# Kernel optimization log

Measured on AMD Instinct MI355X. Metric: run time of the kernel, lower is better.

The kernel has to match this reference:

```python
import math
import jax, jax.numpy as jnp
import numpy as np

N, E = 20000, 640000
S_DIM, Z_DIM, H, QK, VD = 64, 64, 4, 8, 8
EPS = 1e-8


def quat_rotate(v, q):
    # v: [..., 3], q: [..., 4] (w, x, y, z), broadcastable. Unit-quaternion rotation:
    # v' = v + 2*(w*(u x v) + u x (u x v))
    w = q[..., 0:1]
    u = q[..., 1:4]
    uv = jnp.cross(u, v)
    return v + 2.0 * (w * uv + jnp.cross(u, uv))


def setup_inputs() -> dict:
    key = jax.random.key(0)
    ks = jax.random.split(key, 16)
    s = jax.random.normal(ks[0], (N, S_DIM), dtype=jnp.float32)
    z = jax.random.normal(ks[1], (E, Z_DIM), dtype=jnp.float32)
    edge_index = jax.random.randint(ks[2], (2, E), 0, N)
    quaternion = jax.random.normal(ks[3], (N, 4), dtype=jnp.float32)
    quaternion = quaternion / jnp.linalg.norm(quaternion, axis=-1, keepdims=True)
    translation = jax.random.normal(ks[4], (N, 3), dtype=jnp.float32)
    sc_s = 1.0 / math.sqrt(S_DIM)
    sc_z = 1.0 / math.sqrt(Z_DIM)
    # weights stored [in, out] so y = x @ W (equivalent to torch x @ W.T)
    Wq_s = jax.random.normal(ks[5], (S_DIM, H * S_DIM), dtype=jnp.float32) * sc_s
    Wk_s = jax.random.normal(ks[6], (S_DIM, H * S_DIM), dtype=jnp.float32) * sc_s
    Wv_s = jax.random.normal(ks[7], (S_DIM, H * S_DIM), dtype=jnp.float32) * sc_s
    Wq_v = jax.random.normal(ks[8], (S_DIM, H * QK * 3), dtype=jnp.float32) * sc_s
    Wk_v = jax.random.normal(ks[9], (S_DIM, H * QK * 3), dtype=jnp.float32) * sc_s
    Wv_v = jax.random.normal(ks[10], (S_DIM, H * VD * 3), dtype=jnp.float32) * sc_s
    Wb = jax.random.normal(ks[11], (Z_DIM, H), dtype=jnp.float32) * sc_z
    bb = jnp.zeros((H,), dtype=jnp.float32)
    Wdz = jax.random.normal(ks[12], (Z_DIM, Z_DIM // 4), dtype=jnp.float32) * sc_z
    bdz = jnp.zeros((Z_DIM // 4,), dtype=jnp.float32)
    head_weights = jnp.full((H,), 0.541324854612918, dtype=jnp.float32)  # softplus^{-1}(1)
    concat_dim = Z_DIM // 4 + S_DIM + VD * 4
    Wout = jax.random.normal(ks[13], (H * concat_dim, S_DIM), dtype=jnp.float32) / math.sqrt(H * concat_dim)
    bout = jnp.zeros((S_DIM,), dtype=jnp.float32)
    return {
        's': s, 'z': z, 'edge_index': edge_index, 'quaternion': quaternion,
        'translation': translation, 'Wq_s': Wq_s, 'Wk_s': Wk_s, 'Wv_s': Wv_s,
        'Wq_v': Wq_v, 'Wk_v': Wk_v, 'Wv_v': Wv_v, 'Wb': Wb, 'bb': bb,
        'Wdz': Wdz, 'bdz': bdz, 'head_weights': head_weights,
        'Wout': Wout, 'bout': bout,
    }


def reference(s, z, edge_index, quaternion, translation,
              Wq_s, Wk_s, Wv_s, Wq_v, Wk_v, Wv_v,
              Wb, bb, Wdz, bdz, head_weights, Wout, bout):
    idx_i, idx_j = edge_index[0], edge_index[1]
    n = s.shape[0]
    h = head_weights.shape[0]
    qk = Wq_v.shape[1] // (3 * h)
    vd = Wv_v.shape[1] // (3 * h)

    q_scalar = (s @ Wq_s).reshape(n, h, -1)
    k_scalar = (s @ Wk_s).reshape(n, h, -1)
    v_scalar = (s @ Wv_s).reshape(n, h, -1)

    def to_points(x):
        # torch.split into 3 chunks then stack(dim=-1): [n, 3*c] -> [n, c, 3]
        c = x.shape[-1] // 3
        return jnp.swapaxes(x.reshape(n, 3, c), 1, 2)

    quat_b = quaternion[:, None, :]
    trans_b = translation[:, None, :]
    q_vec = (quat_rotate(to_points(s @ Wq_v), quat_b) + trans_b).reshape(n, h, qk, 3)
    k_vec = (quat_rotate(to_points(s @ Wk_v), quat_b) + trans_b).reshape(n, h, qk, 3)
    v_vec = (quat_rotate(to_points(s @ Wv_v), quat_b) + trans_b).reshape(n, h, vd, 3)

    b_bias = z @ Wb + bb  # [E, H]

    attn = jnp.sum(k_scalar[idx_i] * q_scalar[idx_j], axis=-1)  # [E, H]
    attn = attn * math.sqrt(1.0 / 3 * qk) + math.sqrt(1.0 / 3) * b_bias

    disp = q_vec[idx_i] - k_vec[idx_j]            # [E, H, qk, 3]
    vec_att = jnp.sum(disp * disp, axis=-1)       # [E, H, qk]
    hw = jax.nn.softplus(head_weights)[None, :, None]
    vec_att = jnp.sum(vec_att * hw, axis=-1) * math.sqrt(1.0 / (3 * (qk * 9.0 / 2))) * (-0.5)
    attn = attn + vec_att

    # segment softmax over destination node idx_i
    seg_max = jax.ops.segment_max(attn, idx_i, num_segments=n)
    ea = jnp.exp(attn - seg_max[idx_i])
    denom = jax.ops.segment_sum(ea, idx_i, num_segments=n)
    attn = ea / denom[idx_i]                      # [E, H]

    out_scalar = jax.ops.segment_sum(attn[:, :, None] * v_scalar[idx_i], idx_i, num_segments=n)
    out_scalar = out_scalar.reshape(n, -1)

    out_vec = jax.ops.segment_sum(attn[:, :, None, None] * v_vec[idx_i], idx_i, num_segments=n)
    out_vec = out_vec - translation[:, None, None, :]
    q_conj = jnp.concatenate([quaternion[:, :1], -quaternion[:, 1:]], axis=-1)
    out_vec = quat_rotate(out_vec, q_conj[:, None, None, :])   # [n, h, vd, 3]
    out_vec_norm = jnp.sqrt(jnp.sum(out_vec * out_vec, axis=-1) + EPS).reshape(n, -1)
    out_vec_flat = out_vec.reshape(n, -1, 3)

    pair_z = z @ Wdz + bdz                         # [E, z/4]
    out_pair = jax.ops.segment_sum(attn[:, :, None] * pair_z[:, None, :], idx_i, num_segments=n)
    out_pair = out_pair.reshape(n, -1)

    feats = jnp.concatenate([out_scalar,
                             out_vec_flat[..., 0], out_vec_flat[..., 1], out_vec_flat[..., 2],
                             out_vec_norm, out_pair], axis=-1)
    return feats @ Wout + bout
```

## Files before the change

### kernel.cpp

```cpp
#include <hip/hip_runtime.h>
#include <stdint.h>


#define C_SQRT83  1.6329931618554518f
#define C_SQRT13  0.5773502691896258f
#define C_VEC    -0.04811252243246881f

__device__ __forceinline__ unsigned short f2bf(float f){
  unsigned u = __float_as_uint(f);
  u += 0x7fffu + ((u >> 16) & 1u);
  return (unsigned short)(u >> 16);
}
__device__ __forceinline__ unsigned pack2(float a, float b){
  return (unsigned)f2bf(a) | ((unsigned)f2bf(b) << 16);
}
__device__ __forceinline__ float bflo(unsigned u){ return __uint_as_float(u << 16); }
__device__ __forceinline__ float bfhi(unsigned u){ return __uint_as_float(u & 0xffff0000u); }

__device__ __forceinline__ void quat_rot(float w, float ux, float uy, float uz,
                                         float vx, float vy, float vz,
                                         float& ox, float& oy, float& oz){
  float cx = uy*vz - uz*vy;
  float cy = uz*vx - ux*vz;
  float cz = ux*vy - uy*vx;
  float dx = uy*cz - uz*cy;
  float dy = uz*cx - ux*cz;
  float dz = ux*cy - uy*cx;
  ox = vx + 2.f*(w*cx + dx);
  oy = vy + 2.f*(w*cy + dy);
  oz = vz + 2.f*(w*cz + dz);
}


__global__ __launch_bounds__(256) void k_zero(unsigned* __restrict__ counts, int n){
  int g = blockIdx.x*256 + threadIdx.x;
  if (g < n) counts[g] = 0u;
}

__global__ __launch_bounds__(256) void k_count(const int* __restrict__ ei,
                                               unsigned* __restrict__ counts, int ne){
  int e = blockIdx.x*256 + threadIdx.x;
  if (e >= ne) return;
  atomicAdd(&counts[ei[e]], 1u);
}

__global__ __launch_bounds__(256) void k_scan(const unsigned* __restrict__ counts,
                                              unsigned* __restrict__ row_off,
                                              unsigned* __restrict__ cursor, int n){
  __shared__ unsigned part[256];
  int t = threadIdx.x;
  int chunk = (n + 255) >> 8;
  int s0 = t*chunk, s1 = min(s0 + chunk, n);
  unsigned sum = 0;
  for (int k = s0; k < s1; ++k) sum += counts[k];
  part[t] = sum; __syncthreads();
  for (int off = 1; off < 256; off <<= 1){
    unsigned v = (t >= off) ? part[t-off] : 0u;
    __syncthreads();
    part[t] += v;
    __syncthreads();
  }
  unsigned run = (t == 0) ? 0u : part[t-1];
  for (int k = s0; k < s1; ++k){
    row_off[k] = run; cursor[k] = run; run += counts[k];
  }
  if (t == 255) row_off[n] = part[255];
}

__global__ __launch_bounds__(256) void k_fill(const int* __restrict__ ei,
                                              unsigned* __restrict__ cursor,
                                              unsigned* __restrict__ si,
                                              unsigned* __restrict__ sj,
                                              unsigned* __restrict__ se, int ne){
  int e = blockIdx.x*256 + threadIdx.x;
  if (e >= ne) return;
  int i = ei[e];
  unsigned pos = atomicAdd(&cursor[i], 1u);
  si[pos] = (unsigned)i;
  sj[pos] = (unsigned)ei[ne + e];
  se[pos] = (unsigned)e;
}


#define BN 32

__device__ __forceinline__ void pass256(const float* __restrict__ W,
                                        const float st[BN][66], int cg, int sl,
                                        float acc[8][4]){
  #pragma unroll
  for (int i=0;i<8;i++){ acc[i][0]=0.f; acc[i][1]=0.f; acc[i][2]=0.f; acc[i][3]=0.f; }
  #pragma unroll 4
  for (int k = 0; k < 64; ++k){
    const float4 w = *(const float4*)(W + (size_t)k*256 + cg*4);
    #pragma unroll
    for (int i=0;i<8;i++){
      const float sv = st[sl*8+i][k];
      acc[i][0] += sv*w.x; acc[i][1] += sv*w.y; acc[i][2] += sv*w.z; acc[i][3] += sv*w.w;
    }
  }
}

__device__ __forceinline__ void pass96(const float* __restrict__ W,
                                       const float st[BN][66], int cgp, int slp,
                                       float acc[4][4]){
  #pragma unroll
  for (int i=0;i<4;i++){ acc[i][0]=0.f; acc[i][1]=0.f; acc[i][2]=0.f; acc[i][3]=0.f; }
  if (cgp >= 24) return;
  #pragma unroll 4
  for (int k = 0; k < 64; ++k){
    const float4 w = *(const float4*)(W + (size_t)k*96 + cgp*4);
    #pragma unroll
    for (int i=0;i<4;i++){
      const float sv = st[slp*4+i][k];
      acc[i][0] += sv*w.x; acc[i][1] += sv*w.y; acc[i][2] += sv*w.z; acc[i][3] += sv*w.w;
    }
  }
}

__global__ __launch_bounds__(256) void k_proj(
    const float* __restrict__ s, const float* __restrict__ quat, const float* __restrict__ trans,
    const float* __restrict__ Wqs, const float* __restrict__ Wks, const float* __restrict__ Wvs,
    const float* __restrict__ Wqv, const float* __restrict__ Wkv, const float* __restrict__ Wvv,
    unsigned* __restrict__ qs, unsigned* __restrict__ ks, float* __restrict__ vs,
    unsigned* __restrict__ qv, unsigned* __restrict__ kv, float* __restrict__ vv, int n)
{
  __shared__ float st[BN][66];
  __shared__ float pt[BN][97];
  const int tid = threadIdx.x;
  const int node0 = blockIdx.x * BN;

  #pragma unroll
  for (int r = 0; r < 2; ++r){
    const int idx = tid + r*256;
    const int nd = idx >> 4, c4 = idx & 15;
    const int g = node0 + nd;
    float4 v = make_float4(0.f,0.f,0.f,0.f);
    if (g < n) v = *(const float4*)(s + (size_t)g*64 + c4*4);
    st[nd][c4*4+0]=v.x; st[nd][c4*4+1]=v.y; st[nd][c4*4+2]=v.z; st[nd][c4*4+3]=v.w;
  }
  __syncthreads();

  const int cg = tid & 63, sl = tid >> 6;
  const int cgp = tid & 31, slp = tid >> 5;
  float acc[8][4];

  pass256(Wqs, st, cg, sl, acc);
  #pragma unroll
  for (int i=0;i<8;i++){
    const int g = node0 + sl*8 + i;
    if (g < n){
      uint2 u; u.x = pack2(acc[i][0],acc[i][1]); u.y = pack2(acc[i][2],acc[i][3]);
      *(uint2*)(qs + (size_t)g*128 + cg*2) = u;
    }
  }
  pass256(Wks, st, cg, sl, acc);
  #pragma unroll
  for (int i=0;i<8;i++){
    const int g = node0 + sl*8 + i;
    if (g < n){
      uint2 u; u.x = pack2(acc[i][0],acc[i][1]); u.y = pack2(acc[i][2],acc[i][3]);
      *(uint2*)(ks + (size_t)g*128 + cg*2) = u;
    }
  }
  pass256(Wvs, st, cg, sl, acc);
  #pragma unroll
  for (int i=0;i<8;i++){
    const int g = node0 + sl*8 + i;
    if (g < n){
      float4 f; f.x=acc[i][0]; f.y=acc[i][1]; f.z=acc[i][2]; f.w=acc[i][3];
      *(float4*)(vs + (size_t)g*256 + cg*4) = f;
    }
  }

  float pac[4][4];

  pass96(Wqv, st, cgp, slp, pac);
  __syncthreads();
  if (cgp < 24){
    #pragma unroll
    for (int i=0;i<4;i++){
      #pragma unroll
      for (int c=0;c<4;c++) pt[slp*4+i][cgp*4+c] = pac[i][c];
    }
  }
  __syncthreads();
  #pragma unroll
  for (int r = 0; r < 2; ++r){
    const int t2 = tid + r*256;
    const int nd = t2 >> 4, pp = t2 & 15;
    const int g = node0 + nd;
    if (g < n){
      const float4 q4 = *(const float4*)(quat + (size_t)g*4);
      const float tx = trans[(size_t)g*3], ty = trans[(size_t)g*3+1], tz = trans[(size_t)g*3+2];
      float x0,y0,z0,x1,y1,z1;
      quat_rot(q4.x,q4.y,q4.z,q4.w, pt[nd][2*pp],   pt[nd][32+2*pp],   pt[nd][64+2*pp],   x0,y0,z0);
      quat_rot(q4.x,q4.y,q4.z,q4.w, pt[nd][2*pp+1], pt[nd][32+2*pp+1], pt[nd][64+2*pp+1], x1,y1,z1);
      x0+=tx; y0+=ty; z0+=tz; x1+=tx; y1+=ty; z1+=tz;
      unsigned* d = qv + (size_t)g*48 + pp*3;
      d[0] = pack2(x0,y0); d[1] = pack2(z0,x1); d[2] = pack2(y1,z1);
    }
  }

  pass96(Wkv, st, cgp, slp, pac);
  __syncthreads();
  if (cgp < 24){
    #pragma unroll
    for (int i=0;i<4;i++){
      #pragma unroll
      for (int c=0;c<4;c++) pt[slp*4+i][cgp*4+c] = pac[i][c];
    }
  }
  __syncthreads();
  #pragma unroll
  for (int r = 0; r < 2; ++r){
    const int t2 = tid + r*256;
    const int nd = t2 >> 4, pp = t2 & 15;
    const int g = node0 + nd;
    if (g < n){
      const float4 q4 = *(const float4*)(quat + (size_t)g*4);
      const float tx = trans[(size_t)g*3], ty = trans[(size_t)g*3+1], tz = trans[(size_t)g*3+2];
      float x0,y0,z0,x1,y1,z1;
      quat_rot(q4.x,q4.y,q4.z,q4.w, pt[nd][2*pp],   pt[nd][32+2*pp],   pt[nd][64+2*pp],   x0,y0,z0);
      quat_rot(q4.x,q4.y,q4.z,q4.w, pt[nd][2*pp+1], pt[nd][32+2*pp+1], pt[nd][64+2*pp+1], x1,y1,z1);
      x0+=tx; y0+=ty; z0+=tz; x1+=tx; y1+=ty; z1+=tz;
      unsigned* d = kv + (size_t)g*48 + pp*3;
      d[0] = pack2(x0,y0); d[1] = pack2(z0,x1); d[2] = pack2(y1,z1);
    }
  }

  pass96(Wvv, st, cgp, slp, pac);
  __syncthreads();
  if (cgp < 24){
    #pragma unroll
    for (int i=0;i<4;i++){
      #pragma unroll
      for (int c=0;c<4;c++) pt[slp*4+i][cgp*4+c] = pac[i][c];
    }
  }
  __syncthreads();
  #pragma unroll
  for (int r = 0; r < 12; ++r){
    const int idx = tid + r*256;
    const int nd = idx / 96, col = idx - nd*96;
    const int g = node0 + nd;
    if (g < n) vv[(size_t)g*96 + col] = pt[nd][col];
  }
}


__global__ __launch_bounds__(256) void k_edge(
    const float* __restrict__ z,
    const unsigned* __restrict__ si, const unsigned* __restrict__ sj, const unsigned* __restrict__ se,
    const float* __restrict__ Wb,  const float* __restrict__ bb,
    const float* __restrict__ Wdz, const float* __restrict__ bdz,
    const float* __restrict__ hwts,
    const unsigned* __restrict__ qs, const unsigned* __restrict__ ks,
    const unsigned* __restrict__ qv, const unsigned* __restrict__ kv,
    float* __restrict__ logits, unsigned* __restrict__ pz, int ne)
{
  const int p = blockIdx.x*256 + threadIdx.x;
  if (p >= ne) return;
  const unsigned i = si[p], j = sj[p], e = se[p];

  float b4[4];  b4[0]=b4[1]=b4[2]=b4[3]=0.f;
  float pacc[16];
  #pragma unroll
  for (int c=0;c<16;c++) pacc[c]=0.f;
  const float* zr = z + (size_t)e*64;
  #pragma unroll
  for (int k4 = 0; k4 < 16; ++k4){
    const float4 zv = *(const float4*)(zr + 4*k4);
    #pragma unroll
    for (int kk = 0; kk < 4; ++kk){
      const int k = 4*k4 + kk;
      const float zk = (kk==0)?zv.x:((kk==1)?zv.y:((kk==2)?zv.z:zv.w));
      const float4 wb = *(const float4*)(Wb + k*4);
      b4[0]+=zk*wb.x; b4[1]+=zk*wb.y; b4[2]+=zk*wb.z; b4[3]+=zk*wb.w;
      const float* wd = Wdz + k*16;
      const float4 w0=*(const float4*)(wd), w1=*(const float4*)(wd+4),
                   w2=*(const float4*)(wd+8), w3=*(const float4*)(wd+12);
      pacc[ 0]+=zk*w0.x; pacc[ 1]+=zk*w0.y; pacc[ 2]+=zk*w0.z; pacc[ 3]+=zk*w0.w;
      pacc[ 4]+=zk*w1.x; pacc[ 5]+=zk*w1.y; pacc[ 6]+=zk*w1.z; pacc[ 7]+=zk*w1.w;
      pacc[ 8]+=zk*w2.x; pacc[ 9]+=zk*w2.y; pacc[10]+=zk*w2.z; pacc[11]+=zk*w2.w;
      pacc[12]+=zk*w3.x; pacc[13]+=zk*w3.y; pacc[14]+=zk*w3.z; pacc[15]+=zk*w3.w;
    }
  }
  #pragma unroll
  for (int c=0;c<16;c++) pacc[c] += bdz[c];
  { uint4 u0, u1;
    u0.x=pack2(pacc[0],pacc[1]);   u0.y=pack2(pacc[2],pacc[3]);
    u0.z=pack2(pacc[4],pacc[5]);   u0.w=pack2(pacc[6],pacc[7]);
    u1.x=pack2(pacc[8],pacc[9]);   u1.y=pack2(pacc[10],pacc[11]);
    u1.z=pack2(pacc[12],pacc[13]); u1.w=pack2(pacc[14],pacc[15]);
    uint4* d = (uint4*)(pz + (size_t)p*8);
    d[0]=u0; d[1]=u1; }

  const uint4* kr = (const uint4*)(ks + (size_t)i*128);
  const uint4* qr = (const uint4*)(qs + (size_t)j*128);
  float sdot[4];
  #pragma unroll
  for (int h = 0; h < 4; ++h){
    float acc = 0.f;
    #pragma unroll
    for (int c = 0; c < 8; ++c){
      const uint4 a = kr[h*8+c];
      const uint4 b = qr[h*8+c];
      acc += bflo(a.x)*bflo(b.x) + bfhi(a.x)*bfhi(b.x);
      acc += bflo(a.y)*bflo(b.y) + bfhi(a.y)*bfhi(b.y);
      acc += bflo(a.z)*bflo(b.z) + bfhi(a.z)*bfhi(b.z);
      acc += bflo(a.w)*bflo(b.w) + bfhi(a.w)*bfhi(b.w);
    }
    sdot[h] = acc;
  }

  const uint4* qvr = (const uint4*)(qv + (size_t)i*48);
  const uint4* kvr = (const uint4*)(kv + (size_t)j*48);
  float vsum[4];
  #pragma unroll
  for (int h = 0; h < 4; ++h){
    float acc = 0.f;
    #pragma unroll
    for (int c = 0; c < 3; ++c){
      const uint4 a = qvr[h*3+c];
      const uint4 b = kvr[h*3+c];
      float d;
      d = bflo(a.x)-bflo(b.x); acc += d*d;  d = bfhi(a.x)-bfhi(b.x); acc += d*d;
      d = bflo(a.y)-bflo(b.y); acc += d*d;  d = bfhi(a.y)-bfhi(b.y); acc += d*d;
      d = bflo(a.z)-bflo(b.z); acc += d*d;  d = bfhi(a.z)-bfhi(b.z); acc += d*d;
      d = bflo(a.w)-bflo(b.w); acc += d*d;  d = bfhi(a.w)-bfhi(b.w); acc += d*d;
    }
    vsum[h] = acc;
  }

  float4 lg;
  {
    float l[4];
    #pragma unroll
    for (int h = 0; h < 4; ++h){
      const float hw = log1pf(__expf(hwts[h]));
      l[h] = C_SQRT83*sdot[h] + C_SQRT13*(b4[h] + bb[h]) + C_VEC*hw*vsum[h];
    }
    lg.x=l[0]; lg.y=l[1]; lg.z=l[2]; lg.w=l[3];
  }
  *(float4*)(logits + (size_t)p*4) = lg;
}


__global__ __launch_bounds__(256) void k_soft(
    const float* __restrict__ logits, const unsigned* __restrict__ pz,
    const unsigned* __restrict__ row_off, float* __restrict__ out_pair, int n)
{
  const int t = blockIdx.x*256 + threadIdx.x;
  if (t >= n*4) return;
  const int i = t >> 2, h = t & 3;
  const int beg = (int)row_off[i], end = (int)row_off[i+1];

  float m = -3.4e38f;
  for (int p = beg; p < end; ++p) m = fmaxf(m, logits[(size_t)p*4 + h]);

  float ssum = 0.f;
  float acc[16];
  #pragma unroll
  for (int c=0;c<16;c++) acc[c]=0.f;

  for (int p = beg; p < end; ++p){
    const float w = __expf(logits[(size_t)p*4 + h] - m);
    ssum += w;
    const uint4* pr = (const uint4*)(pz + (size_t)p*8);
    const uint4 a = pr[0], b = pr[1];
    acc[ 0]+=w*bflo(a.x); acc[ 1]+=w*bfhi(a.x);
    acc[ 2]+=w*bflo(a.y); acc[ 3]+=w*bfhi(a.y);
    acc[ 4]+=w*bflo(a.z); acc[ 5]+=w*bfhi(a.z);
    acc[ 6]+=w*bflo(a.w); acc[ 7]+=w*bfhi(a.w);
    acc[ 8]+=w*bflo(b.x); acc[ 9]+=w*bfhi(b.x);
    acc[10]+=w*bflo(b.y); acc[11]+=w*bfhi(b.y);
    acc[12]+=w*bflo(b.z); acc[13]+=w*bfhi(b.z);
    acc[14]+=w*bflo(b.w); acc[15]+=w*bfhi(b.w);
  }
  const float inv = (end > beg) ? (1.f/ssum) : 0.f;
  float4* dst = (float4*)(out_pair + (size_t)i*64 + h*16);
  float4 o;
  o.x=acc[0]*inv;  o.y=acc[1]*inv;  o.z=acc[2]*inv;  o.w=acc[3]*inv;  dst[0]=o;
  o.x=acc[4]*inv;  o.y=acc[5]*inv;  o.z=acc[6]*inv;  o.w=acc[7]*inv;  dst[1]=o;
  o.x=acc[8]*inv;  o.y=acc[9]*inv;  o.z=acc[10]*inv; o.w=acc[11]*inv; dst[2]=o;
  o.x=acc[12]*inv; o.y=acc[13]*inv; o.z=acc[14]*inv; o.w=acc[15]*inv; dst[3]=o;
}


__global__ __launch_bounds__(256) void k_out(
    const float* __restrict__ vs, const float* __restrict__ vv,
    const float* __restrict__ out_pair, const unsigned* __restrict__ row_off,
    const float* __restrict__ quat, const float* __restrict__ trans,
    const float* __restrict__ Wout, const float* __restrict__ bout,
    float* __restrict__ out, int n)
{
  __shared__ float feats[32][448];
  __shared__ int degs[32];
  const int tid = threadIdx.x;
  const int node0 = blockIdx.x*32;

  if (tid < 32){
    const int g = node0 + tid;
    degs[tid] = (g < n) ? (int)(row_off[g+1] - row_off[g]) : 1;
  }
  __syncthreads();

  for (int x = tid; x < 32*256; x += 256){
    const int nd = x >> 8, c = x & 255;
    const int g = node0 + nd;
    feats[nd][c] = (g < n && degs[nd] > 0) ? vs[(size_t)g*256 + c] : 0.f;
  }
  for (int x = tid; x < 32*64; x += 256){
    const int nd = x >> 6, c = x & 63;
    const int g = node0 + nd;
    feats[nd][384 + c] = (g < n) ? out_pair[(size_t)g*64 + c] : 0.f;
  }
  for (int x = tid; x < 32*32; x += 256){
    const int nd = x >> 5, pt = x & 31;
    const int g = node0 + nd;
    float X=0.f, Y=0.f, Z=0.f;
    if (g < n){
      if (degs[nd] > 0){
        X = vv[(size_t)g*96 + pt];
        Y = vv[(size_t)g*96 + 32 + pt];
        Z = vv[(size_t)g*96 + 64 + pt];
      } else {
        const float4 q4 = *(const float4*)(quat + (size_t)g*4);
        const float tx = trans[(size_t)g*3], ty = trans[(size_t)g*3+1], tz = trans[(size_t)g*3+2];
        quat_rot(q4.x, -q4.y, -q4.z, -q4.w, -tx, -ty, -tz, X, Y, Z);
      }
    }
    feats[nd][256 + pt] = X;
    feats[nd][288 + pt] = Y;
    feats[nd][320 + pt] = Z;
    feats[nd][352 + pt] = sqrtf(X*X + Y*Y + Z*Z + 1e-8f);
  }
  __syncthreads();

  const int lane = tid & 63;
  const int wave = tid >> 6;
  float acc[8];
  #pragma unroll
  for (int q8=0;q8<8;q8++) acc[q8]=0.f;

  for (int k = 0; k < 448; ++k){
    const float wv = Wout[(size_t)k*64 + lane];
    #pragma unroll
    for (int q8 = 0; q8 < 8; ++q8)
      acc[q8] += feats[wave*8 + q8][k] * wv;
  }
  const float bo = bout[lane];
  #pragma unroll
  for (int q8 = 0; q8 < 8; ++q8){
    const int g = node0 + wave*8 + q8;
    if (g < n) out[(size_t)g*64 + lane] = acc[q8] + bo;
  }
}


extern "C" void kernel_launch(void* const* d_in, const int* in_sizes, int n_in,
                              void* d_out, int out_size, void* d_ws, size_t ws_size,
                              hipStream_t stream) {
  const float* s     = (const float*)d_in[0];
  const float* z     = (const float*)d_in[1];
  const int*   ei    = (const int*)  d_in[2];
  const float* quat  = (const float*)d_in[3];
  const float* trans = (const float*)d_in[4];
  const float* Wqs   = (const float*)d_in[5];
  const float* Wks   = (const float*)d_in[6];
  const float* Wvs   = (const float*)d_in[7];
  const float* Wqv   = (const float*)d_in[8];
  const float* Wkv   = (const float*)d_in[9];
  const float* Wvv   = (const float*)d_in[10];
  const float* Wb    = (const float*)d_in[11];
  const float* bb    = (const float*)d_in[12];
  const float* Wdz   = (const float*)d_in[13];
  const float* bdz   = (const float*)d_in[14];
  const float* hwts  = (const float*)d_in[15];
  const float* Wout  = (const float*)d_in[16];
  const float* bout  = (const float*)d_in[17];
  float* out = (float*)d_out;

  const int n  = in_sizes[0] / 64;
  const int ne = in_sizes[1] / 64;

  size_t off = 0;
  char* base = (char*)d_ws;
  auto take = [&](size_t bytes)->char* {
    char* p = base + off;
    off += (bytes + 255) & ~(size_t)255;
    return p;
  };
  unsigned* qs     = (unsigned*)take((size_t)n*512);
  unsigned* ks     = (unsigned*)take((size_t)n*512);
  unsigned* qvt    = (unsigned*)take((size_t)n*192);
  unsigned* kvt    = (unsigned*)take((size_t)n*192);
  float*    vs     = (float*)   take((size_t)n*1024);
  float*    vv     = (float*)   take((size_t)n*384);
  float*    logits = (float*)   take((size_t)ne*16);
  unsigned* pz     = (unsigned*)take((size_t)ne*32);
  unsigned* counts = (unsigned*)take((size_t)n*4);
  unsigned* roff   = (unsigned*)take((size_t)(n+1)*4);
  unsigned* cur    = (unsigned*)take((size_t)n*4);
  unsigned* si     = (unsigned*)take((size_t)ne*4);
  unsigned* sj     = (unsigned*)take((size_t)ne*4);
  unsigned* se     = (unsigned*)take((size_t)ne*4);
  float*    opair  = (float*)   take((size_t)n*256);
  (void)ws_size; (void)n_in; (void)out_size;

  const int gbE = (ne + 255) / 256;
  const int gbN = (n  + 255) / 256;

  k_zero <<<gbN, 256, 0, stream>>>(counts, n);
  k_count<<<gbE, 256, 0, stream>>>(ei, counts, ne);
  k_scan <<<1,   256, 0, stream>>>(counts, roff, cur, n);
  k_fill <<<gbE, 256, 0, stream>>>(ei, cur, si, sj, se, ne);
  k_proj <<<(n + BN - 1)/BN, 256, 0, stream>>>(s, quat, trans, Wqs, Wks, Wvs, Wqv, Wkv, Wvv,
                                               qs, ks, vs, qvt, kvt, vv, n);
  k_edge <<<gbE, 256, 0, stream>>>(z, si, sj, se, Wb, bb, Wdz, bdz, hwts,
                                   qs, ks, qvt, kvt, logits, pz, ne);
  k_soft <<<(n*4 + 255)/256, 256, 0, stream>>>(logits, pz, roff, opair, n);
  k_out  <<<(n + 31)/32, 256, 0, stream>>>(vs, vv, opair, roff, quat, trans,
                                           Wout, bout, out, n);
}
```

Measured before the change: 688.1 us.

## Fuse edge logits and segment softmax into one wave-per-node kernel

Replaces the per-edge logit kernel and the per-node softmax kernel with a single kernel where each wavefront handles one destination node. It computes edge logits and pair projections in registers and shared memory, then does an online softmax accumulation. This removes the global logits and pair buffers and the si array, and loads the node's own k/q-vec rows once into shared memory. It also transposes the shared-memory input tile in the projection kernel and vectorizes feature reads in the output kernel. The risks are load imbalance on high-degree nodes, underused waves on low-degree nodes, and reliance on __threadfence_block instead of a barrier for intra-wave shared-memory ordering.

```diff
diff --git a/kernel.cpp b/kernel.cpp
--- a/kernel.cpp
+++ b/kernel.cpp
@@ -69,14 +69,12 @@
 
 __global__ __launch_bounds__(256) void k_fill(const int* __restrict__ ei,
                                               unsigned* __restrict__ cursor,
-                                              unsigned* __restrict__ si,
                                               unsigned* __restrict__ sj,
                                               unsigned* __restrict__ se, int ne){
   int e = blockIdx.x*256 + threadIdx.x;
   if (e >= ne) return;
   int i = ei[e];
   unsigned pos = atomicAdd(&cursor[i], 1u);
-  si[pos] = (unsigned)i;
   sj[pos] = (unsigned)ei[ne + e];
   se[pos] = (unsigned)e;
 }
@@ -85,23 +83,28 @@
 #define BN 32
 
 __device__ __forceinline__ void pass256(const float* __restrict__ W,
-                                        const float st[BN][66], int cg, int sl,
+                                        const float stT[64][40], int cg, int sl,
                                         float acc[8][4]){
   #pragma unroll
   for (int i=0;i<8;i++){ acc[i][0]=0.f; acc[i][1]=0.f; acc[i][2]=0.f; acc[i][3]=0.f; }
   #pragma unroll 4
   for (int k = 0; k < 64; ++k){
-    const float4 w = *(const float4*)(W + (size_t)k*256 + cg*4);
-    #pragma unroll
-    for (int i=0;i<8;i++){
-      const float sv = st[sl*8+i][k];
-      acc[i][0] += sv*w.x; acc[i][1] += sv*w.y; acc[i][2] += sv*w.z; acc[i][3] += sv*w.w;
-    }
+    const float4 w  = *(const float4*)(W + (size_t)k*256 + cg*4);
+    const float4 n0 = *(const float4*)&stT[k][sl*8];
+    const float4 n1 = *(const float4*)&stT[k][sl*8+4];
+    acc[0][0]+=n0.x*w.x; acc[0][1]+=n0.x*w.y; acc[0][2]+=n0.x*w.z; acc[0][3]+=n0.x*w.w;
+    acc[1][0]+=n0.y*w.x; acc[1][1]+=n0.y*w.y; acc[1][2]+=n0.y*w.z; acc[1][3]+=n0.y*w.w;
+    acc[2][0]+=n0.z*w.x; acc[2][1]+=n0.z*w.y; acc[2][2]+=n0.z*w.z; acc[2][3]+=n0.z*w.w;
+    acc[3][0]+=n0.w*w.x; acc[3][1]+=n0.w*w.y; acc[3][2]+=n0.w*w.z; acc[3][3]+=n0.w*w.w;
+    acc[4][0]+=n1.x*w.x; acc[4][1]+=n1.x*w.y; acc[4][2]+=n1.x*w.z; acc[4][3]+=n1.x*w.w;
+    acc[5][0]+=n1.y*w.x; acc[5][1]+=n1.y*w.y; acc[5][2]+=n1.y*w.z; acc[5][3]+=n1.y*w.w;
+    acc[6][0]+=n1.z*w.x; acc[6][1]+=n1.z*w.y; acc[6][2]+=n1.z*w.z; acc[6][3]+=n1.z*w.w;
+    acc[7][0]+=n1.w*w.x; acc[7][1]+=n1.w*w.y; acc[7][2]+=n1.w*w.z; acc[7][3]+=n1.w*w.w;
   }
 }
 
 __device__ __forceinline__ void pass96(const float* __restrict__ W,
-                                       const float st[BN][66], int cgp, int slp,
+                                       const float stT[64][40], int cgp, int slp,
                                        float acc[4][4]){
   #pragma unroll
   for (int i=0;i<4;i++){ acc[i][0]=0.f; acc[i][1]=0.f; acc[i][2]=0.f; acc[i][3]=0.f; }
@@ -109,11 +112,11 @@
   #pragma unroll 4
   for (int k = 0; k < 64; ++k){
     const float4 w = *(const float4*)(W + (size_t)k*96 + cgp*4);
-    #pragma unroll
-    for (int i=0;i<4;i++){
-      const float sv = st[slp*4+i][k];
-      acc[i][0] += sv*w.x; acc[i][1] += sv*w.y; acc[i][2] += sv*w.z; acc[i][3] += sv*w.w;
-    }
+    const float4 nv = *(const float4*)&stT[k][slp*4];
+    acc[0][0]+=nv.x*w.x; acc[0][1]+=nv.x*w.y; acc[0][2]+=nv.x*w.z; acc[0][3]+=nv.x*w.w;
+    acc[1][0]+=nv.y*w.x; acc[1][1]+=nv.y*w.y; acc[1][2]+=nv.y*w.z; acc[1][3]+=nv.y*w.w;
+    acc[2][0]+=nv.z*w.x; acc[2][1]+=nv.z*w.y; acc[2][2]+=nv.z*w.z; acc[2][3]+=nv.z*w.w;
+    acc[3][0]+=nv.w*w.x; acc[3][1]+=nv.w*w.y; acc[3][2]+=nv.w*w.z; acc[3][3]+=nv.w*w.w;
   }
 }
 
@@ -124,7 +127,7 @@
     unsigned* __restrict__ qs, unsigned* __restrict__ ks, float* __restrict__ vs,
     unsigned* __restrict__ qv, unsigned* __restrict__ kv, float* __restrict__ vv, int n)
 {
-  __shared__ float st[BN][66];
+  __shared__ float stT[64][40];
   __shared__ float pt[BN][97];
   const int tid = threadIdx.x;
   const int node0 = blockIdx.x * BN;
@@ -136,7 +139,7 @@
     const int g = node0 + nd;
     float4 v = make_float4(0.f,0.f,0.f,0.f);
     if (g < n) v = *(const float4*)(s + (size_t)g*64 + c4*4);
-    st[nd][c4*4+0]=v.x; st[nd][c4*4+1]=v.y; st[nd][c4*4+2]=v.z; st[nd][c4*4+3]=v.w;
+    stT[c4*4+0][nd]=v.x; stT[c4*4+1][nd]=v.y; stT[c4*4+2][nd]=v.z; stT[c4*4+3][nd]=v.w;
   }
   __syncthreads();
 
@@ -144,7 +147,7 @@
   const int cgp = tid & 31, slp = tid >> 5;
   float acc[8][4];
 
-  pass256(Wqs, st, cg, sl, acc);
+  pass256(Wqs, stT, cg, sl, acc);
   #pragma unroll
   for (int i=0;i<8;i++){
     const int g = node0 + sl*8 + i;
@@ -153,7 +156,7 @@
       *(uint2*)(qs + (size_t)g*128 + cg*2) = u;
     }
   }
-  pass256(Wks, st, cg, sl, acc);
+  pass256(Wks, stT, cg, sl, acc);
   #pragma unroll
   for (int i=0;i<8;i++){
     const int g = node0 + sl*8 + i;
@@ -162,7 +165,7 @@
       *(uint2*)(ks + (size_t)g*128 + cg*2) = u;
     }
   }
-  pass256(Wvs, st, cg, sl, acc);
+  pass256(Wvs, stT, cg, sl, acc);
   #pragma unroll
   for (int i=0;i<8;i++){
     const int g = node0 + sl*8 + i;
@@ -174,7 +177,7 @@
 
   float pac[4][4];
 
-  pass96(Wqv, st, cgp, slp, pac);
+  pass96(Wqv, stT, cgp, slp, pac);
   __syncthreads();
   if (cgp < 24){
     #pragma unroll
@@ -201,7 +204,7 @@
     }
   }
 
-  pass96(Wkv, st, cgp, slp, pac);
+  pass96(Wkv, stT, cgp, slp, pac);
   __syncthreads();
   if (cgp < 24){
     #pragma unroll
@@ -228,7 +231,7 @@
     }
   }
 
-  pass96(Wvv, st, cgp, slp, pac);
+  pass96(Wvv, stT, cgp, slp, pac);
   __syncthreads();
   if (cgp < 24){
     #pragma unroll
@@ -248,142 +251,153 @@
 }
 
 
-__global__ __launch_bounds__(256) void k_edge(
+__global__ __launch_bounds__(256) void k_seg(
     const float* __restrict__ z,
-    const unsigned* __restrict__ si, const unsigned* __restrict__ sj, const unsigned* __restrict__ se,
+    const unsigned* __restrict__ sj, const unsigned* __restrict__ se,
+    const unsigned* __restrict__ row_off,
     const float* __restrict__ Wb,  const float* __restrict__ bb,
     const float* __restrict__ Wdz, const float* __restrict__ bdz,
     const float* __restrict__ hwts,
-    const unsigned* __restrict__ qs, const unsigned* __restrict__ ks,
+    const unsigned* __restrict__ qs, const unsigned* __restrict__ ksc,
     const unsigned* __restrict__ qv, const unsigned* __restrict__ kv,
-    float* __restrict__ logits, unsigned* __restrict__ pz, int ne)
+    float* __restrict__ out_pair, int n)
 {
-  const int p = blockIdx.x*256 + threadIdx.x;
-  if (p >= ne) return;
-  const unsigned i = si[p], j = sj[p], e = se[p];
-
-  float b4[4];  b4[0]=b4[1]=b4[2]=b4[3]=0.f;
-  float pacc[16];
-  #pragma unroll
-  for (int c=0;c<16;c++) pacc[c]=0.f;
-  const float* zr = z + (size_t)e*64;
-  #pragma unroll
-  for (int k4 = 0; k4 < 16; ++k4){
-    const float4 zv = *(const float4*)(zr + 4*k4);
-    #pragma unroll
-    for (int kk = 0; kk < 4; ++kk){
-      const int k = 4*k4 + kk;
-      const float zk = (kk==0)?zv.x:((kk==1)?zv.y:((kk==2)?zv.z:zv.w));
-      const float4 wb = *(const float4*)(Wb + k*4);
-      b4[0]+=zk*wb.x; b4[1]+=zk*wb.y; b4[2]+=zk*wb.z; b4[3]+=zk*wb.w;
-      const float* wd = Wdz + k*16;
-      const float4 w0=*(const float4*)(wd), w1=*(const float4*)(wd+4),
-                   w2=*(const float4*)(wd+8), w3=*(const float4*)(wd+12);
-      pacc[ 0]+=zk*w0.x; pacc[ 1]+=zk*w0.y; pacc[ 2]+=zk*w0.z; pacc[ 3]+=zk*w0.w;
-      pacc[ 4]+=zk*w1.x; pacc[ 5]+=zk*w1.y; pacc[ 6]+=zk*w1.z; pacc[ 7]+=zk*w1.w;
-      pacc[ 8]+=zk*w2.x; pacc[ 9]+=zk*w2.y; pacc[10]+=zk*w2.z; pacc[11]+=zk*w2.w;
-      pacc[12]+=zk*w3.x; pacc[13]+=zk*w3.y; pacc[14]+=zk*w3.z; pacc[15]+=zk*w3.w;
-    }
-  }
-  #pragma unroll
-  for (int c=0;c<16;c++) pacc[c] += bdz[c];
-  { uint4 u0, u1;
-    u0.x=pack2(pacc[0],pacc[1]);   u0.y=pack2(pacc[2],pacc[3]);
-    u0.z=pack2(pacc[4],pacc[5]);   u0.w=pack2(pacc[6],pacc[7]);
-    u1.x=pack2(pacc[8],pacc[9]);   u1.y=pack2(pacc[10],pacc[11]);
-    u1.z=pack2(pacc[12],pacc[13]); u1.w=pack2(pacc[14],pacc[15]);
-    uint4* d = (uint4*)(pz + (size_t)p*8);
-    d[0]=u0; d[1]=u1; }
-
-  const uint4* kr = (const uint4*)(ks + (size_t)i*128);
-  const uint4* qr = (const uint4*)(qs + (size_t)j*128);
-  float sdot[4];
-  #pragma unroll
-  for (int h = 0; h < 4; ++h){
-    float acc = 0.f;
-    #pragma unroll
-    for (int c = 0; c < 8; ++c){
-      const uint4 a = kr[h*8+c];
-      const uint4 b = qr[h*8+c];
-      acc += bflo(a.x)*bflo(b.x) + bfhi(a.x)*bfhi(b.x);
-      acc += bflo(a.y)*bflo(b.y) + bfhi(a.y)*bfhi(b.y);
-      acc += bflo(a.z)*bflo(b.z) + bfhi(a.z)*bfhi(b.z);
-      acc += bflo(a.w)*bflo(b.w) + bfhi(a.w)*bfhi(b.w);
-    }
-    sdot[h] = acc;
-  }
-
-  const uint4* qvr = (const uint4*)(qv + (size_t)i*48);
-  const uint4* kvr = (const uint4*)(kv + (size_t)j*48);
-  float vsum[4];
-  #pragma unroll
-  for (int h = 0; h < 4; ++h){
-    float acc = 0.f;
-    #pragma unroll
-    for (int c = 0; c < 3; ++c){
-      const uint4 a = qvr[h*3+c];
-      const uint4 b = kvr[h*3+c];
-      float d;
-      d = bflo(a.x)-bflo(b.x); acc += d*d;  d = bfhi(a.x)-bfhi(b.x); acc += d*d;
-      d = bflo(a.y)-bflo(b.y); acc += d*d;  d = bfhi(a.y)-bfhi(b.y); acc += d*d;
-      d = bflo(a.z)-bflo(b.z); acc += d*d;  d = bfhi(a.z)-bfhi(b.z); acc += d*d;
-      d = bflo(a.w)-bflo(b.w); acc += d*d;  d = bfhi(a.w)-bfhi(b.w); acc += d*d;
-    }
-    vsum[h] = acc;
-  }
-
-  float4 lg;
-  {
-    float l[4];
+  __shared__ uint4    sh_ks[4][32];
+  __shared__ uint4    sh_qv[4][12];
+  __shared__ float    sh_l [4][64][4];
+  __shared__ unsigned sh_pz[4][64][8];
+
+  const int wv   = threadIdx.x >> 6;
+  const int lane = threadIdx.x & 63;
+  const int node = blockIdx.x*4 + wv;
+  if (node >= n) return;
+
+  const int beg = (int)row_off[node], end = (int)row_off[node+1];
+
+  if (lane < 32)      sh_ks[wv][lane]    = ((const uint4*)(ksc + (size_t)node*128))[lane];
+  else if (lane < 44) sh_qv[wv][lane-32] = ((const uint4*)(qv  + (size_t)node*48))[lane-32];
+  __threadfence_block();
+
+  float hwv[4];
+  #pragma unroll
+  for (int h=0;h<4;h++) hwv[h] = C_VEC * log1pf(__expf(hwts[h]));
+
+  const int hl = lane >> 4, cl = lane & 15;
+  float m4[4] = {-3.0e38f,-3.0e38f,-3.0e38f,-3.0e38f};
+  float accO = 0.f, S = 0.f;
+
+  for (int base = beg; base < end; base += 64){
+    const int p = base + lane;
+    const bool act = (p < end);
+    const unsigned j = act ? sj[p] : 0u;
+    const unsigned e = act ? se[p] : 0u;
+
+    float b4[4]; float pz[16];
+    b4[0]=bb[0]; b4[1]=bb[1]; b4[2]=bb[2]; b4[3]=bb[3];
+    #pragma unroll
+    for (int c=0;c<16;c++) pz[c] = bdz[c];
+    const float4* zr = (const float4*)(z + (size_t)e*64);
+    #pragma unroll 4
+    for (int k4 = 0; k4 < 16; ++k4){
+      const float4 zv = zr[k4];
+      const float zk[4] = {zv.x, zv.y, zv.z, zv.w};
+      #pragma unroll
+      for (int kk = 0; kk < 4; ++kk){
+        const int k = k4*4 + kk;
+        const float zs = zk[kk];
+        #pragma unroll
+        for (int c=0;c<4;c++)  b4[c] += zs * Wb[k*4+c];
+        #pragma unroll
+        for (int c=0;c<16;c++) pz[c] += zs * Wdz[k*16+c];
+      }
+    }
+
+    const uint4* qj = (const uint4*)(qs + (size_t)j*128);
+    float sdot[4];
     #pragma unroll
     for (int h = 0; h < 4; ++h){
-      const float hw = log1pf(__expf(hwts[h]));
-      l[h] = C_SQRT83*sdot[h] + C_SQRT13*(b4[h] + bb[h]) + C_VEC*hw*vsum[h];
-    }
-    lg.x=l[0]; lg.y=l[1]; lg.z=l[2]; lg.w=l[3];
-  }
-  *(float4*)(logits + (size_t)p*4) = lg;
-}
-
-
-__global__ __launch_bounds__(256) void k_soft(
-    const float* __restrict__ logits, const unsigned* __restrict__ pz,
-    const unsigned* __restrict__ row_off, float* __restrict__ out_pair, int n)
-{
-  const int t = blockIdx.x*256 + threadIdx.x;
-  if (t >= n*4) return;
-  const int i = t >> 2, h = t & 3;
-  const int beg = (int)row_off[i], end = (int)row_off[i+1];
-
-  float m = -3.4e38f;
-  for (int p = beg; p < end; ++p) m = fmaxf(m, logits[(size_t)p*4 + h]);
-
-  float ssum = 0.f;
-  float acc[16];
-  #pragma unroll
-  for (int c=0;c<16;c++) acc[c]=0.f;
-
-  for (int p = beg; p < end; ++p){
-    const float w = __expf(logits[(size_t)p*4 + h] - m);
-    ssum += w;
-    const uint4* pr = (const uint4*)(pz + (size_t)p*8);
-    const uint4 a = pr[0], b = pr[1];
-    acc[ 0]+=w*bflo(a.x); acc[ 1]+=w*bfhi(a.x);
-    acc[ 2]+=w*bflo(a.y); acc[ 3]+=w*bfhi(a.y);
-    acc[ 4]+=w*bflo(a.z); acc[ 5]+=w*bfhi(a.z);
-    acc[ 6]+=w*bflo(a.w); acc[ 7]+=w*bfhi(a.w);
-    acc[ 8]+=w*bflo(b.x); acc[ 9]+=w*bfhi(b.x);
-    acc[10]+=w*bflo(b.y); acc[11]+=w*bfhi(b.y);
-    acc[12]+=w*bflo(b.z); acc[13]+=w*bfhi(b.z);
-    acc[14]+=w*bflo(b.w); acc[15]+=w*bfhi(b.w);
-  }
-  const float inv = (end > beg) ? (1.f/ssum) : 0.f;
-  float4* dst = (float4*)(out_pair + (size_t)i*64 + h*16);
-  float4 o;
-  o.x=acc[0]*inv;  o.y=acc[1]*inv;  o.z=acc[2]*inv;  o.w=acc[3]*inv;  dst[0]=o;
-  o.x=acc[4]*inv;  o.y=acc[5]*inv;  o.z=acc[6]*inv;  o.w=acc[7]*inv;  dst[1]=o;
-  o.x=acc[8]*inv;  o.y=acc[9]*inv;  o.z=acc[10]*inv; o.w=acc[11]*inv; dst[2]=o;
-  o.x=acc[12]*inv; o.y=acc[13]*inv; o.z=acc[14]*inv; o.w=acc[15]*inv; dst[3]=o;
+      uint4 qb[8];
+      #pragma unroll
+      for (int c=0;c<8;c++) qb[c] = qj[h*8+c];
+      float acc = 0.f;
+      #pragma unroll
+      for (int c=0;c<8;c++){
+        const uint4 a = sh_ks[wv][h*8+c];
+        const uint4 b = qb[c];
+        acc += bflo(a.x)*bflo(b.x) + bfhi(a.x)*bfhi(b.x);
+        acc += bflo(a.y)*bflo(b.y) + bfhi(a.y)*bfhi(b.y);
+        acc += bflo(a.z)*bflo(b.z) + bfhi(a.z)*bfhi(b.z);
+        acc += bflo(a.w)*bflo(b.w) + bfhi(a.w)*bfhi(b.w);
+      }
+      sdot[h] = acc;
+    }
+
+    const uint4* kj = (const uint4*)(kv + (size_t)j*48);
+    float vsum[4];
+    #pragma unroll
+    for (int h = 0; h < 4; ++h){
+      uint4 kb[3];
+      #pragma unroll
+      for (int c=0;c<3;c++) kb[c] = kj[h*3+c];
+      float acc = 0.f, d;
+      #pragma unroll
+      for (int c=0;c<3;c++){
+        const uint4 a = sh_qv[wv][h*3+c];
+        const uint4 b = kb[c];
+        d=bflo(a.x)-bflo(b.x); acc+=d*d; d=bfhi(a.x)-bfhi(b.x); acc+=d*d;
+        d=bflo(a.y)-bflo(b.y); acc+=d*d; d=bfhi(a.y)-bfhi(b.y); acc+=d*d;
+        d=bflo(a.z)-bflo(b.z); acc+=d*d; d=bfhi(a.z)-bfhi(b.z); acc+=d*d;
+        d=bflo(a.w)-bflo(b.w); acc+=d*d; d=bfhi(a.w)-bfhi(b.w); acc+=d*d;
+      }
+      vsum[h] = acc;
+    }
+
+    float l4[4];
+    #pragma unroll
+    for (int h = 0; h < 4; ++h)
+      l4[h] = act ? (C_SQRT83*sdot[h] + C_SQRT13*b4[h] + hwv[h]*vsum[h]) : -3.0e38f;
+
+    *(float4*)&sh_l[wv][lane][0] = make_float4(l4[0], l4[1], l4[2], l4[3]);
+    {
+      uint4 u0, u1;
+      u0.x=pack2(pz[0],pz[1]);   u0.y=pack2(pz[2],pz[3]);
+      u0.z=pack2(pz[4],pz[5]);   u0.w=pack2(pz[6],pz[7]);
+      u1.x=pack2(pz[8],pz[9]);   u1.y=pack2(pz[10],pz[11]);
+      u1.z=pack2(pz[12],pz[13]); u1.w=pack2(pz[14],pz[15]);
+      uint4* d = (uint4*)&sh_pz[wv][lane][0];
+      d[0]=u0; d[1]=u1;
+    }
+
+    float cm[4] = {l4[0], l4[1], l4[2], l4[3]};
+    #pragma unroll
+    for (int msk = 1; msk < 64; msk <<= 1){
+      #pragma unroll
+      for (int h=0;h<4;h++) cm[h] = fmaxf(cm[h], __shfl_xor(cm[h], msk));
+    }
+    float mn[4];
+    #pragma unroll
+    for (int h=0;h<4;h++) mn[h] = fmaxf(m4[h], cm[h]);
+    const float scale = __expf(m4[hl] - mn[hl]);
+    accO *= scale; S *= scale;
+    #pragma unroll
+    for (int h=0;h<4;h++) m4[h] = mn[h];
+
+    __threadfence_block();
+
+    const int cnt = min(64, end - base);
+    const float mh = m4[hl];
+    for (int p2 = 0; p2 < cnt; ++p2){
+      const float w = __expf(sh_l[wv][p2][hl] - mh);
+      S += w;
+      const unsigned u = sh_pz[wv][p2][cl>>1];
+      const float pzv = (cl & 1) ? bfhi(u) : bflo(u);
+      accO += w * pzv;
+    }
+    __threadfence_block();
+  }
+
+  const float inv = (S > 0.f) ? (1.f/S) : 0.f;
+  out_pair[(size_t)node*64 + lane] = accO * inv;
 }
 
 
@@ -443,11 +457,16 @@
   #pragma unroll
   for (int q8=0;q8<8;q8++) acc[q8]=0.f;
 
-  for (int k = 0; k < 448; ++k){
-    const float wv = Wout[(size_t)k*64 + lane];
-    #pragma unroll
-    for (int q8 = 0; q8 < 8; ++q8)
-      acc[q8] += feats[wave*8 + q8][k] * wv;
+  for (int k0 = 0; k0 < 448; k0 += 4){
+    const float w0 = Wout[(size_t)(k0+0)*64 + lane];
+    const float w1 = Wout[(size_t)(k0+1)*64 + lane];
+    const float w2 = Wout[(size_t)(k0+2)*64 + lane];
+    const float w3 = Wout[(size_t)(k0+3)*64 + lane];
+    #pragma unroll
+    for (int q8 = 0; q8 < 8; ++q8){
+      const float4 f = *(const float4*)&feats[wave*8 + q8][k0];
+      acc[q8] += f.x*w0 + f.y*w1 + f.z*w2 + f.w*w3;
+    }
   }
   const float bo = bout[lane];
   #pragma unroll
@@ -497,12 +516,9 @@
   unsigned* kvt    = (unsigned*)take((size_t)n*192);
   float*    vs     = (float*)   take((size_t)n*1024);
   float*    vv     = (float*)   take((size_t)n*384);
-  float*    logits = (float*)   take((size_t)ne*16);
-  unsigned* pz     = (unsigned*)take((size_t)ne*32);
   unsigned* counts = (unsigned*)take((size_t)n*4);
   unsigned* roff   = (unsigned*)take((size_t)(n+1)*4);
   unsigned* cur    = (unsigned*)take((size_t)n*4);
-  unsigned* si     = (unsigned*)take((size_t)ne*4);
   unsigned* sj     = (unsigned*)take((size_t)ne*4);
   unsigned* se     = (unsigned*)take((size_t)ne*4);
   float*    opair  = (float*)   take((size_t)n*256);
@@ -514,12 +530,11 @@
   k_zero <<<gbN, 256, 0, stream>>>(counts, n);
   k_count<<<gbE, 256, 0, stream>>>(ei, counts, ne);
   k_scan <<<1,   256, 0, stream>>>(counts, roff, cur, n);
-  k_fill <<<gbE, 256, 0, stream>>>(ei, cur, si, sj, se, ne);
+  k_fill <<<gbE, 256, 0, stream>>>(ei, cur, sj, se, ne);
   k_proj <<<(n + BN - 1)/BN, 256, 0, stream>>>(s, quat, trans, Wqs, Wks, Wvs, Wqv, Wkv, Wvv,
                                                qs, ks, vs, qvt, kvt, vv, n);
-  k_edge <<<gbE, 256, 0, stream>>>(z, si, sj, se, Wb, bb, Wdz, bdz, hwts,
-                                   qs, ks, qvt, kvt, logits, pz, ne);
-  k_soft <<<(n*4 + 255)/256, 256, 0, stream>>>(logits, pz, roff, opair, n);
+  k_seg  <<<(n + 3)/4, 256, 0, stream>>>(z, sj, se, roff, Wb, bb, Wdz, bdz, hwts,
+                                         qs, ks, qvt, kvt, opair, n);
   k_out  <<<(n + 31)/32, 256, 0, stream>>>(vs, vv, opair, roff, quat, trans,
                                            Wout, bout, out, n);
 }
```

New measurement: 807.0 us. 1.17x slower.
